# Kernel tuning notes

Hardware: AMD Instinct MI355X
Metric: run time of the kernel (lower is better)

## Reference

```python
import jax, jax.numpy as jnp
import numpy as np

B, S, F, H, A = 256, 128, 512, 1024, 18


def setup_inputs() -> dict:
    key = jax.random.key(0)
    ks = jax.random.split(key, 16)
    u = lambda k, shape, fan: jax.random.uniform(k, shape, jnp.float32, -1.0, 1.0) / np.sqrt(fan)
    return {
        "obs": jax.random.normal(ks[0], (B, S, F), jnp.float32),
        "hx": jax.random.normal(ks[1], (B, H), jnp.float32),
        "cx": jax.random.normal(ks[2], (B, H), jnp.float32),
        "behaviour_acts": jax.random.randint(ks[3], (B, S, 1), 0, A),
        "W1": u(ks[4], (H, F), F), "b1": u(ks[5], (H,), F),
        "W_ih": u(ks[6], (4 * H, H), H), "b_ih": u(ks[7], (4 * H,), H),
        "W_hh": u(ks[8], (4 * H, H), H), "b_hh": u(ks[9], (4 * H,), H),
        "W_v": u(ks[10], (1, H), H), "b_v": u(ks[11], (1,), H),
        "W_l": u(ks[12], (A, H), H), "b_l": u(ks[13], (A,), H),
    }


def reference(obs, hx, cx, behaviour_acts, W1, b1, W_ih, b_ih, W_hh, b_hh, W_v, b_v, W_l, b_l):
    # MLP body: [B,S,F] -> [B,S,H]
    x = jax.nn.relu(jnp.einsum("bsf,hf->bsh", obs, W1) + b1)
    # precompute input-to-gate projection for all timesteps (one big GEMM)
    xg = jnp.einsum("bsh,gh->bsg", x, W_ih) + b_ih  # [B,S,4H]

    def step(carry, xg_t):
        h, c = carry
        gates = xg_t + h @ W_hh.T + b_hh  # [B,4H], gate order i,f,g,o (torch LSTMCell)
        i, f, g, o = jnp.split(gates, 4, axis=-1)
        c = jax.nn.sigmoid(f) * c + jax.nn.sigmoid(i) * jnp.tanh(g)
        h = jax.nn.sigmoid(o) * jnp.tanh(c)
        return (h, c), h

    _, hs = jax.lax.scan(step, (hx, cx), jnp.swapaxes(xg, 0, 1))
    output = jnp.swapaxes(hs, 0, 1)  # [B,S,H]

    value = output @ W_v.T + b_v  # [B,S,1]
    logits = output @ W_l.T + b_l  # [B,S,A]
    # torch Categorical(probs=softmax(logits)) => log-prob via log_softmax
    logp = jax.nn.log_softmax(logits, axis=-1)
    acts = behaviour_acts.reshape(logits.shape[0], logits.shape[1], 1)
    log_probs = jnp.take_along_axis(logp, acts, axis=-1)  # [B,S,1]
    entropy = -jnp.sum(jnp.exp(logp) * logp, axis=-1, keepdims=True)  # [B,S,1]
    return log_probs, entropy, value
```

## Files before the change

kernel.cpp:

```cpp
#include <hip/hip_runtime.h>

#define B_ 256
#define S_ 128
#define F_ 512
#define H_ 1024
#define A_ 18
#define M_ (B_*S_)
#define G_ (4*H_)
#define CH_ 16
#define CR_ (B_*CH_)

typedef unsigned short u16;
typedef __attribute__((ext_vector_type(8))) _Float16 f16x8;
typedef __attribute__((ext_vector_type(4))) _Float16 f16x4;
typedef __attribute__((ext_vector_type(8))) short   s16x8;
typedef __attribute__((ext_vector_type(4))) float f32x4;
typedef __attribute__((ext_vector_type(4))) unsigned int u32x4;

__device__ __forceinline__ float bf2f(u16 u){
  union{unsigned int i; float f;} v; v.i=((unsigned int)u)<<16; return v.f;
}
__device__ __forceinline__ u16 f2bf(float f){
  unsigned int i=__float_as_uint(f);
  unsigned int r=(i+0x7fffu+((i>>16)&1u))>>16;
  return (u16)r;
}
__device__ __forceinline__ u16 f2h(float f){
  _Float16 h=(_Float16)f;
  union{_Float16 h; u16 u;} v; v.h=h; return v.u;
}
__device__ __forceinline__ float ldf(const void* p, size_t i, int m){
  return m ? ((const float*)p)[i] : bf2f(((const u16*)p)[i]);
}
__device__ __forceinline__ f16x8 load8_h(const void* base, size_t off, int m){
  f16x8 v;
  if(m==2) return *(const f16x8*)((const u16*)base + off);
  if(m==1){
    const float* f=(const float*)base + off;
    float4 a=*(const float4*)f; float4 b=*(const float4*)(f+4);
    v[0]=(_Float16)a.x; v[1]=(_Float16)a.y; v[2]=(_Float16)a.z; v[3]=(_Float16)a.w;
    v[4]=(_Float16)b.x; v[5]=(_Float16)b.y; v[6]=(_Float16)b.z; v[7]=(_Float16)b.w;
    return v;
  }
  s16x8 w=*(const s16x8*)((const u16*)base + off);
#pragma unroll
  for(int k=0;k<8;k++) v[k]=(_Float16)bf2f((u16)w[k]);
  return v;
}

__device__ __forceinline__ u32x4 load_c16(const void* p){
  u32x4 r;
  asm volatile("global_load_dwordx4 %0, %1, off sc0 sc1" : "=v"(r) : "v"(p));
  return r;
}
__device__ __forceinline__ void store_c2(u16* p, u16 v){
  unsigned int vv=v;
  asm volatile("global_store_short %0, %1, off sc0 sc1" :: "v"(p), "v"(vv) : "memory");
}
__device__ __forceinline__ int load_c4(const int* p){
  int r;
  asm volatile("global_load_dword %0, %1, off sc0 sc1" : "=v"(r) : "v"(p));
  return r;
}
__device__ __forceinline__ void store_c4(int* p, int v){
  asm volatile("global_store_dword %0, %1, off sc0 sc1" :: "v"(p), "v"(v) : "memory");
}

__device__ __forceinline__ void bar_flags32(int* flags, int target, int gi, int lane, int w){
  asm volatile("s_waitcnt vmcnt(0)" ::: "memory");
  __syncthreads();
  if(w==0){
    if(lane==0) store_c4(flags+gi, target);
    while(true){
      int v=load_c4(flags+(lane&31));
      asm volatile("s_waitcnt vmcnt(0)" ::: "memory");
      if(__all(v>=target)) break;
      __builtin_amdgcn_s_sleep(1);
    }
  }
  __syncthreads();
}

template<int ROWS, int MAP>
__device__ __forceinline__ void stage(const void* base, int mode, int lda, int k0,
                                      int rowoff, int t0, u16* lds, int tid){
  if(mode==2){
    constexpr int NI=(ROWS*8)/256;
    int wv=tid>>6, l=tid&63;
#pragma unroll
    for(int i=0;i<NI;i++){
      int s0=i*256+(wv<<6), s=s0+l;
      int r=s>>3, gc=(s&7)^(r&7);
      int p=rowoff+r, sr;
      if(MAP==0)      sr=p;
      else if(MAP==1) sr=(p&3)*H_+(p>>2);
      else            sr=(p>>4)*S_+t0+(p&15);
      const u16* src=(const u16*)base + (size_t)sr*lda + k0 + gc*8;
      u16* dst=lds + s0*8;
      __builtin_amdgcn_global_load_lds((const __attribute__((address_space(1))) unsigned int*)src,
                                       (__attribute__((address_space(3))) unsigned int*)dst,
                                       16, 0, 0);
    }
  } else {
#pragma unroll
    for(int s0=tid; s0<ROWS*8; s0+=256){
      int r=s0>>3, gc=s0&7, lc=gc^(r&7);
      int p=rowoff+r, sr;
      if(MAP==0)      sr=p;
      else if(MAP==1) sr=(p&3)*H_+(p>>2);
      else            sr=(p>>4)*S_+t0+(p&15);
      f16x8 v=load8_h(base, (size_t)sr*lda + k0 + gc*8, mode);
      *(f16x8*)(lds + r*64 + lc*8)=v;
    }
  }
}

__device__ __forceinline__ f16x8 frag_ld(const u16* lds, int r0, int kc, int lane){
  int r = r0 + (lane&15);
  int c = (kc + (lane>>4)) ^ (r&7);
  return *(const f16x8*)(lds + r*64 + c*8);
}

template<int AMAP, int BMAP, int OUTMODE>
__global__ __launch_bounds__(256,3) void gemm128(const void* A, const void* Bt, void* C,
    const float* __restrict__ biasf, const int* __restrict__ flag,
    int K, int lda, int ldb, int ldc, int t0, int amode, int bmode){
  int m=*flag;
  int am = amode<0 ? m : amode;
  int bm_ = bmode<0 ? m : bmode;
  __shared__ u16 As[128*64];
  __shared__ u16 Bs[128*64];
  int tid=threadIdx.x, lane=tid&63, w=tid>>6;
  int bm=blockIdx.y*128, bn=blockIdx.x*128;
  int wm=(w&1)*64, wn=(w>>1)*64;
  f32x4 acc[4][4];
#pragma unroll
  for(int i=0;i<4;i++)
#pragma unroll
    for(int j=0;j<4;j++) acc[i][j]=(f32x4)(0.f);
  for(int k0=0;k0<K;k0+=64){
    stage<128,AMAP>(A , am,  lda, k0, bm, t0, As, tid);
    stage<128,BMAP>(Bt, bm_, ldb, k0, bn, t0, Bs, tid);
    __syncthreads();
#pragma unroll
    for(int kk=0;kk<2;kk++){
      f16x8 af[4], bq[4];
#pragma unroll
      for(int i=0;i<4;i++) af[i]=frag_ld(As, wm+i*16, kk*4, lane);
#pragma unroll
      for(int j=0;j<4;j++) bq[j]=frag_ld(Bs, wn+j*16, kk*4, lane);
#pragma unroll
      for(int i=0;i<4;i++)
#pragma unroll
        for(int j=0;j<4;j++)
          acc[i][j]=__builtin_amdgcn_mfma_f32_16x16x32_f16(af[i],bq[j],acc[i][j],0,0,0);
    }
    __syncthreads();
  }
  int rl=lane>>4, cl=lane&15;
#pragma unroll
  for(int j=0;j<4;j++){
    int col=bn+wn+j*16+cl;
    float bb=biasf[col];
#pragma unroll
    for(int i=0;i<4;i++){
#pragma unroll
      for(int r=0;r<4;r++){
        int row=bm+wm+i*16+rl*4+r;
        float v=acc[i][j][r]+bb;
        if(OUTMODE==0){ v=fmaxf(v,0.f); ((u16*)C)[(size_t)row*ldc+col]=f2h(v); }
        else if(OUTMODE==2){ ((u16*)C)[(size_t)row*ldc+col]=f2h(v); }
        else { ((float*)C)[(size_t)row*ldc+col]=v; }
      }
    }
  }
}

__global__ __launch_bounds__(512,2) void lstm_persist(u16* __restrict__ hh,
        const u16* __restrict__ Whhp, const u16* __restrict__ xgp,
        float* __restrict__ cst, int* __restrict__ cntc, int tbase){
  __shared__ u16 As[16*2048];
  __shared__ float gs[32*132];
  int tid=threadIdx.x, lane=tid&63, w=tid>>6;
  int grp=blockIdx.x&7, ci=blockIdx.x>>3;
  int bm=grp*32, bn=ci*128;
  int* flags = cntc + grp*64;

  f16x8 bw[32];
#pragma unroll
  for(int t=0;t<32;t++){
    int p = bn + w*16 + (lane&15);
    int k = t*32 + (lane>>4)*8;
    bw[t]=*(const f16x8*)(Whhp + (size_t)p*H_ + k);
  }
#pragma unroll
  for(int t=0;t<32;t++) asm volatile("" : "+a"(bw[t]));

  int rl0=tid>>5, rl1=(tid+512)>>5, u0=tid&31;
  int gu=(bn>>2)+u0;
  float c0=cst[(size_t)(bm+rl0)*H_+gu];
  float c1=cst[(size_t)(bm+rl1)*H_+gu];

  for(int dt=0;dt<CH_;dt++){
    f16x4 xv0=*(const f16x4*)(xgp + ((size_t)(bm+rl0)*CH_+dt)*G_ + bn + u0*4);
    f16x4 xv1=*(const f16x4*)(xgp + ((size_t)(bm+rl1)*CH_+dt)*G_ + bn + u0*4);
    if(dt) bar_flags32(flags, tbase+dt, ci, lane, w);
    {
      int slotPrev=(dt+CH_-1)&(CH_-1);
      u32x4 tmp[8];
#pragma unroll
      for(int i=0;i<8;i++){
        int s=tid+i*512, kt=s>>8, r=(s>>3)&31, gc=s&7;
        tmp[i]=load_c16(hh + ((size_t)(bm+r)*CH_+slotPrev)*H_ + kt*64 + gc*8);
      }
      asm volatile("s_waitcnt vmcnt(0)" ::: "memory");
#pragma unroll
      for(int i=0;i<8;i++){
        int s=tid+i*512, kt=s>>8, r=(s>>3)&31, gc=s&7, lc=gc^(r&7);
        *(u32x4*)(As + kt*2048 + r*64 + lc*8)=tmp[i];
      }
    }
    __syncthreads();
    f32x4 acc0=(f32x4)(0.f), acc1=(f32x4)(0.f);
#pragma unroll
    for(int t=0;t<32;t++){
      int kt=t>>1, kk=t&1;
      f16x8 af0=frag_ld(As+kt*2048, 0,  kk*4, lane);
      f16x8 af1=frag_ld(As+kt*2048, 16, kk*4, lane);
      acc0=__builtin_amdgcn_mfma_f32_16x16x32_f16(af0,bw[t],acc0,0,0,0);
      acc1=__builtin_amdgcn_mfma_f32_16x16x32_f16(af1,bw[t],acc1,0,0,0);
    }
#pragma unroll
    for(int r=0;r<4;r++){
      gs[(   (lane>>4)*4+r)*132 + w*16+(lane&15)]=acc0[r];
      gs[(16+(lane>>4)*4+r)*132 + w*16+(lane&15)]=acc1[r];
    }
    __syncthreads();
    {
      float4 gv=*(const float4*)&gs[rl0*132+u0*4];
      float ii=1.f/(1.f+__expf(-(gv.x+(float)xv0[0])));
      float ff=1.f/(1.f+__expf(-(gv.y+(float)xv0[1])));
      float gg=1.f-2.f/(__expf(2.f*(gv.z+(float)xv0[2]))+1.f);
      float oo=1.f/(1.f+__expf(-(gv.w+(float)xv0[3])));
      c0=ff*c0+ii*gg;
      float th=1.f-2.f/(__expf(2.f*c0)+1.f);
      store_c2(hh + ((size_t)(bm+rl0)*CH_+dt)*H_ + gu, f2h(oo*th));
    }
    {
      float4 gv=*(const float4*)&gs[rl1*132+u0*4];
      float ii=1.f/(1.f+__expf(-(gv.x+(float)xv1[0])));
      float ff=1.f/(1.f+__expf(-(gv.y+(float)xv1[1])));
      float gg=1.f-2.f/(__expf(2.f*(gv.z+(float)xv1[2]))+1.f);
      float oo=1.f/(1.f+__expf(-(gv.w+(float)xv1[3])));
      c1=ff*c1+ii*gg;
      float th=1.f-2.f/(__expf(2.f*c1)+1.f);
      store_c2(hh + ((size_t)(bm+rl1)*CH_+dt)*H_ + gu, f2h(oo*th));
    }
  }
  cst[(size_t)(bm+rl0)*H_+gu]=c0;
  cst[(size_t)(bm+rl1)*H_+gu]=c1;
}

__global__ __launch_bounds__(256,2) void lstm_step(u16* __restrict__ hh, int slotPrev, int dt,
        const void* __restrict__ Whh, const u16* __restrict__ xg,
        float* __restrict__ cst, const int* __restrict__ flag){
  int m=*flag;
  __shared__ u16 As[64*64];
  __shared__ u16 Bs[64*64];
  __shared__ float gs[64*64];
  int tid=threadIdx.x, lane=tid&63, w=tid>>6;
  int bm=blockIdx.y*64, bn=blockIdx.x*64;
  int wm=(w&1)*32, wn=(w>>1)*32;
  f32x4 acc[2][2];
#pragma unroll
  for(int i=0;i<2;i++)
#pragma unroll
    for(int j=0;j<2;j++) acc[i][j]=(f32x4)(0.f);
  for(int k0=0;k0<H_;k0+=64){
    stage<64,0>(hh + slotPrev*H_, 2, CH_*H_, k0, bm, 0, As, tid);
    stage<64,1>(Whh,              m, H_,     k0, bn, 0, Bs, tid);
    __syncthreads();
#pragma unroll
    for(int kk=0;kk<2;kk++){
      f16x8 af[2], bq[2];
#pragma unroll
      for(int i=0;i<2;i++) af[i]=frag_ld(As, wm+i*16, kk*4, lane);
#pragma unroll
      for(int j=0;j<2;j++) bq[j]=frag_ld(Bs, wn+j*16, kk*4, lane);
#pragma unroll
      for(int i=0;i<2;i++)
#pragma unroll
        for(int j=0;j<2;j++)
          acc[i][j]=__builtin_amdgcn_mfma_f32_16x16x32_f16(af[i],bq[j],acc[i][j],0,0,0);
    }
    __syncthreads();
  }
  int rl=lane>>4, cl=lane&15;
#pragma unroll
  for(int j=0;j<2;j++){
    int coll=wn+j*16+cl;
#pragma unroll
    for(int i=0;i<2;i++){
#pragma unroll
      for(int r=0;r<4;r++){
        int rowl=wm+i*16+rl*4+r;
        float xv=(float)((const _Float16*)xg)[((size_t)(bm+rowl)*CH_+dt)*G_ + bn+coll];
        gs[rowl*64+coll]=acc[i][j][r] + xv;
      }
    }
  }
  __syncthreads();
#pragma unroll
  for(int p=0;p<4;p++){
    int idx=p*256+tid;
    int rowl=idx>>4, u=idx&15;
    float4 gv = *(const float4*)&gs[rowl*64+u*4];
    float ii=1.f/(1.f+__expf(-gv.x));
    float ff=1.f/(1.f+__expf(-gv.y));
    float gg=1.f-2.f/(__expf(2.f*gv.z)+1.f);
    float oo=1.f/(1.f+__expf(-gv.w));
    int gb=bm+rowl;
    int gu=(bn>>2)+u;
    size_t ci=(size_t)gb*H_+gu;
    float cn=ff*cst[ci]+ii*gg;
    cst[ci]=cn;
    float th=1.f-2.f/(__expf(2.f*cn)+1.f);
    hh[(size_t)gb*(CH_*H_) + dt*H_ + gu]=f2h(oo*th);
  }
}

__global__ __launch_bounds__(256,2) void heads_chunk(const u16* __restrict__ hh,
      const void* __restrict__ Wl, const void* __restrict__ Wv,
      const float* __restrict__ blf, const int* __restrict__ acts,
      void* __restrict__ out, const int* __restrict__ flag, int t0){
  int m=*flag;
  int rg = blockIdx.x*4 + (threadIdx.x>>6);
  int lane = threadIdx.x & 63;
  const u16* h = hh + (size_t)rg*H_;
  u32x4 hv0=load_c16(h + lane*16);
  u32x4 hv1=load_c16(h + lane*16 + 8);
  f16x8 h0=__builtin_bit_cast(f16x8,hv0), h1=__builtin_bit_cast(f16x8,hv1);
  float hv[16];
#pragma unroll
  for(int k=0;k<8;k++){ hv[k]=(float)h0[k]; hv[8+k]=(float)h1[k]; }
  float dots[19];
#pragma unroll
  for(int j=0;j<19;j++){
    const void* wrow = (j<18) ? Wl : Wv;
    size_t roff = (j<18) ? (size_t)j*H_ : 0;
    float wv_[16];
    if(m){
      const float* f=(const float*)wrow + roff + lane*16;
      float4 a=*(const float4*)f, b=*(const float4*)(f+4), c=*(const float4*)(f+8), d=*(const float4*)(f+12);
      wv_[0]=a.x;wv_[1]=a.y;wv_[2]=a.z;wv_[3]=a.w; wv_[4]=b.x;wv_[5]=b.y;wv_[6]=b.z;wv_[7]=b.w;
      wv_[8]=c.x;wv_[9]=c.y;wv_[10]=c.z;wv_[11]=c.w; wv_[12]=d.x;wv_[13]=d.y;wv_[14]=d.z;wv_[15]=d.w;
    } else {
      const u16* ub=(const u16*)wrow + roff + lane*16;
      s16x8 w0=*(const s16x8*)ub, w1=*(const s16x8*)(ub+8);
#pragma unroll
      for(int k=0;k<8;k++){ wv_[k]=bf2f((u16)w0[k]); wv_[8+k]=bf2f((u16)w1[k]); }
    }
    float d=0.f;
#pragma unroll
    for(int k=0;k<16;k++) d += hv[k]*wv_[k];
#pragma unroll
    for(int mm=1;mm<64;mm<<=1) d += __shfl_xor(d, mm, 64);
    dots[j]=d;
  }
  float lg[18];
#pragma unroll
  for(int j=0;j<18;j++) lg[j]=dots[j]+blf[j];
  float value=dots[18]+blf[18];
  float mx=lg[0];
#pragma unroll
  for(int j=1;j<18;j++) mx=fmaxf(mx,lg[j]);
  float se=0.f, s1=0.f;
#pragma unroll
  for(int j=0;j<18;j++){ float e=__expf(lg[j]-mx); se+=e; s1+=e*(lg[j]-mx); }
  float lse=__logf(se);
  int b=rg>>4, dt=rg&(CH_-1);
  int gw = b*S_ + t0 + dt;
  int a=acts[gw];
  float la=0.f;
#pragma unroll
  for(int j=0;j<18;j++) la = (j==a) ? lg[j] : la;
  float lp=la-mx-lse;
  float ent=lse - s1/se;
  if(lane==0){
    if(m){
      ((float*)out)[gw]=lp; ((float*)out)[M_+gw]=ent; ((float*)out)[2*M_+gw]=value;
    } else {
      ((u16*)out)[gw]=f2bf(lp); ((u16*)out)[M_+gw]=f2bf(ent); ((u16*)out)[2*M_+gw]=f2bf(value);
    }
  }
}

__global__ void detect(const u16* __restrict__ obs_w, int* __restrict__ flag){
  __shared__ float red[256];
  float mx=0.f;
  for(int i=threadIdx.x;i<4096;i+=256) mx=fmaxf(mx,fabsf(bf2f(obs_w[i])));
  red[threadIdx.x]=mx; __syncthreads();
  for(int s=128;s>0;s>>=1){
    if(threadIdx.x<s) red[threadIdx.x]=fmaxf(red[threadIdx.x],red[threadIdx.x+s]);
    __syncthreads();
  }
  if(threadIdx.x==0) *flag=(red[0]>1e4f)?1:0;
}

__global__ void prep(const void* bih, const void* bhh, const void* b1, const void* bl, const void* bv,
                     const void* cx, const void* hx,
                     float* biasg, float* b1f, float* blf, float* cst, u16* hh,
                     int* cnt, const int* __restrict__ flag){
  int m=*flag;
  size_t i=(size_t)blockIdx.x*256+threadIdx.x;
  if(i<G_){ size_t rm=(i&3)*H_+(i>>2); biasg[i]=ldf(bih,rm,m)+ldf(bhh,rm,m); return; }
  i-=G_;
  if(i<H_){ b1f[i]=ldf(b1,i,m); return; }
  i-=H_;
  if(i<19){ blf[i]=(i<18)?ldf(bl,i,m):ldf(bv,0,m); return; }
  i-=19;
  if(i<512){ cnt[i]=0; return; }
  i-=512;
  if(i<(size_t)B_*H_){ cst[i]=ldf(cx,i,m); return; }
  i-=(size_t)B_*H_;
  if(i<(size_t)B_*H_){
    size_t b=i>>10, k=i&1023;
    hh[b*(CH_*H_) + (CH_-1)*H_ + k]=f2h(ldf(hx,i,m));
  }
}

__global__ void convw(const void* W1, const void* Wih, const void* Whh,
                      u16* W1h, u16* Wihp, u16* Whhp, const int* __restrict__ flag){
  int m=*flag;
  size_t i=((size_t)blockIdx.x*256+threadIdx.x)*8;
  const size_t n1=(size_t)H_*F_, n2=(size_t)G_*H_;
  if(i<n1){ *(f16x8*)(W1h+i)=load8_h(W1,i,m); return; }
  i-=n1;
  if(i<n2){ size_t p=i>>10, c=i&1023; size_t sr=(p&3)*H_+(p>>2);
            *(f16x8*)(Wihp+i)=load8_h(Wih, sr*H_+c, m); return; }
  i-=n2;
  if(i<n2){ size_t p=i>>10, c=i&1023; size_t sr=(p&3)*H_+(p>>2);
            *(f16x8*)(Whhp+i)=load8_h(Whh, sr*H_+c, m); return; }
}
__global__ void convobs(const void* obs, u16* obsh, const int* __restrict__ flag){
  int m=*flag;
  size_t i=((size_t)blockIdx.x*256+threadIdx.x)*8;
  if(i<(size_t)M_*F_) *(f16x8*)(obsh+i)=load8_h(obs,i,m);
}

extern "C" void kernel_launch(void* const* d_in, const int* in_sizes, int n_in,
                              void* d_out, int out_size, void* d_ws, size_t ws_size,
                              hipStream_t stream){
  const void* obs=d_in[0];
  const void* hx =d_in[1];
  const void* cx =d_in[2];
  const int* acts=(const int*)d_in[3];
  const void* W1 =d_in[4];
  const void* b1 =d_in[5];
  const void* Wih=d_in[6];
  const void* bih=d_in[7];
  const void* Whh=d_in[8];
  const void* bhh=d_in[9];
  const void* Wv =d_in[10];
  const void* bv =d_in[11];
  const void* Wl =d_in[12];
  const void* bl =d_in[13];

  char* w=(char*)d_ws;
  auto alloc=[&](size_t n){ char* p=w; w+=((n+255)&~(size_t)255); return p; };
  int*   flag =(int*)alloc(4);
  int*   cnt  =(int*)alloc(512*4);
  float* biasg=(float*)alloc((size_t)G_*4);
  float* b1f  =(float*)alloc((size_t)H_*4);
  float* blf  =(float*)alloc(32*4);
  float* cst  =(float*)alloc((size_t)B_*H_*4);
  u16*   hh   =(u16*)alloc((size_t)B_*CH_*H_*2);
  u16*   xc   =(u16*)alloc((size_t)CR_*H_*2);
  u16*   xg   =(u16*)alloc((size_t)CR_*G_*2);
  size_t nW=((size_t)H_*F_ + 2*(size_t)G_*H_)*2 + 768;
  bool pathW = ((size_t)(w-(char*)d_ws) + nW) <= ws_size;
  u16 *W1h=0,*Wihp=0,*Whhp=0;
  if(pathW){ W1h=(u16*)alloc((size_t)H_*F_*2); Wihp=(u16*)alloc((size_t)G_*H_*2); Whhp=(u16*)alloc((size_t)G_*H_*2); }
  size_t nXC=(size_t)M_*H_*2 + 256;
  bool pathXC = pathW && (((size_t)(w-(char*)d_ws) + nXC) <= ws_size);
  u16* xcf=0; if(pathXC) xcf=(u16*)alloc((size_t)M_*H_*2);
  size_t nO=(size_t)M_*F_*2 + 256;
  bool pathO = pathXC && (((size_t)(w-(char*)d_ws) + nO) <= ws_size);
  u16* obsh=0; if(pathO) obsh=(u16*)alloc((size_t)M_*F_*2);

  detect<<<1,256,0,stream>>>((const u16*)obs, flag);
  {
    int total=G_+H_+19+512+B_*H_+B_*H_;
    prep<<<(total+255)/256,256,0,stream>>>(bih,bhh,b1,bl,bv,cx,hx, biasg,b1f,blf,cst,hh,cnt, flag);
  }
  if(pathW){
    size_t n=((size_t)H_*F_+2*(size_t)G_*H_)/8;
    convw<<<(int)((n+255)/256),256,0,stream>>>(W1,Wih,Whh, W1h,Wihp,Whhp, flag);
  }
  if(pathO){
    size_t n=(size_t)M_*F_/8;
    convobs<<<(int)((n+255)/256),256,0,stream>>>(obs, obsh, flag);
  }
  if(pathXC){
    gemm128<0,0,0><<<dim3(H_/128, M_/128),256,0,stream>>>(
        pathO?(const void*)obsh:obs, pathW?(const void*)W1h:W1, xcf, b1f, flag,
        F_, F_, F_, H_, 0, pathO?2:-1, pathW?2:-1);
  }

  for(int c=0;c<S_/CH_;c++){
    int t0=c*CH_;
    if(!pathXC){
      gemm128<2,0,0><<<dim3(H_/128, CR_/128),256,0,stream>>>(
          obs, pathW?(const void*)W1h:W1, xc, b1f, flag, F_, F_, F_, H_, t0, -1, pathW?2:-1);
    }
    if(pathXC)
      gemm128<2,0,2><<<dim3(G_/128, CR_/128),256,0,stream>>>(
          xcf, Wihp, xg, biasg, flag, H_, H_, H_, G_, t0, 2, 2);
    else if(pathW)
      gemm128<0,0,2><<<dim3(G_/128, CR_/128),256,0,stream>>>(
          xc, Wihp, xg, biasg, flag, H_, H_, H_, G_, 0, 2, 2);
    else
      gemm128<0,1,2><<<dim3(G_/128, CR_/128),256,0,stream>>>(
          xc, Wih, xg, biasg, flag, H_, H_, H_, G_, 0, 2, -1);

    if(pathW)
      lstm_persist<<<256,512,0,stream>>>(hh, Whhp, xg, cst, cnt, t0);
    else
      for(int dt=0;dt<CH_;dt++)
        lstm_step<<<dim3(G_/64, B_/64),256,0,stream>>>(hh, (dt+CH_-1)&(CH_-1), dt, Whh, xg, cst, flag);

    heads_chunk<<<dim3(CR_/4),256,0,stream>>>(hh, Wl, Wv, blf, acts, d_out, flag, t0);
  }
}
```

Measured before the change: 1.220 ms.

## Reorganize persistent LSTM step: register gate layout, split barrier, prefetch xg

The MFMA operand order is swapped so each lane's accumulator holds the four gates of one hidden unit. This removes the LDS round trip through the gate buffer and one block barrier per timestep. The grid barrier is split: each block publishes its flag right after storing its h slice, and waits on the others only at the top of the next step. The next step's xg values are prefetched after the flag is published. The h loads now use ordinary cached loads instead of sc0/sc1 coherent loads, with even/odd accumulators added for MFMA ILP. The cost is an extra small LDS transpose before the h stores, and a risk that plain loads read stale h values from other blocks.

```diff
diff --git a/kernel.cpp b/kernel.cpp
--- a/kernel.cpp
+++ b/kernel.cpp
@@ -64,21 +64,6 @@
 }
 __device__ __forceinline__ void store_c4(int* p, int v){
   asm volatile("global_store_dword %0, %1, off sc0 sc1" :: "v"(p), "v"(v) : "memory");
-}
-
-__device__ __forceinline__ void bar_flags32(int* flags, int target, int gi, int lane, int w){
-  asm volatile("s_waitcnt vmcnt(0)" ::: "memory");
-  __syncthreads();
-  if(w==0){
-    if(lane==0) store_c4(flags+gi, target);
-    while(true){
-      int v=load_c4(flags+(lane&31));
-      asm volatile("s_waitcnt vmcnt(0)" ::: "memory");
-      if(__all(v>=target)) break;
-      __builtin_amdgcn_s_sleep(1);
-    }
-  }
-  __syncthreads();
 }
 
 template<int ROWS, int MAP>
@@ -180,7 +165,7 @@
         const u16* __restrict__ Whhp, const u16* __restrict__ xgp,
         float* __restrict__ cst, int* __restrict__ cntc, int tbase){
   __shared__ u16 As[16*2048];
-  __shared__ float gs[32*132];
+  __shared__ u16 hs[32*36];
   int tid=threadIdx.x, lane=tid&63, w=tid>>6;
   int grp=blockIdx.x&7, ci=blockIdx.x>>3;
   int bm=grp*32, bn=ci*128;
@@ -196,24 +181,40 @@
 #pragma unroll
   for(int t=0;t<32;t++) asm volatile("" : "+a"(bw[t]));
 
-  int rl0=tid>>5, rl1=(tid+512)>>5, u0=tid&31;
-  int gu=(bn>>2)+u0;
-  float c0=cst[(size_t)(bm+rl0)*H_+gu];
-  float c1=cst[(size_t)(bm+rl1)*H_+gu];
+  int bb0=lane&15, bb1=16+(lane&15);
+  int ul = w*4 + (lane>>4);
+  int gu2 = (bn>>2) + ul;
+  float c0=cst[(size_t)(bm+bb0)*H_+gu2];
+  float c1=cst[(size_t)(bm+bb1)*H_+gu2];
+  int sb0=tid>>5, su=tid&31, sb1=(tid+512)>>5;
+
+  size_t xoff0=((size_t)(bm+bb0)*CH_)*G_ + bn + w*16 + (lane>>4)*4;
+  size_t xoff1=((size_t)(bm+bb1)*CH_)*G_ + bn + w*16 + (lane>>4)*4;
+  f16x4 xga0=*(const f16x4*)(xgp + xoff0);
+  f16x4 xga1=*(const f16x4*)(xgp + xoff1);
 
   for(int dt=0;dt<CH_;dt++){
-    f16x4 xv0=*(const f16x4*)(xgp + ((size_t)(bm+rl0)*CH_+dt)*G_ + bn + u0*4);
-    f16x4 xv1=*(const f16x4*)(xgp + ((size_t)(bm+rl1)*CH_+dt)*G_ + bn + u0*4);
-    if(dt) bar_flags32(flags, tbase+dt, ci, lane, w);
+    if(dt){
+      if(w==0){
+        int target=tbase+dt;
+        while(true){
+          int v=load_c4(flags+(lane&31));
+          asm volatile("s_waitcnt vmcnt(0)" ::: "memory");
+          if(__all(v>=target)) break;
+          __builtin_amdgcn_s_sleep(1);
+        }
+      }
+      __syncthreads();
+    }
     {
       int slotPrev=(dt+CH_-1)&(CH_-1);
+      const u16* hbase = hh + (size_t)slotPrev*H_;
       u32x4 tmp[8];
 #pragma unroll
       for(int i=0;i<8;i++){
         int s=tid+i*512, kt=s>>8, r=(s>>3)&31, gc=s&7;
-        tmp[i]=load_c16(hh + ((size_t)(bm+r)*CH_+slotPrev)*H_ + kt*64 + gc*8);
+        tmp[i]=*(const u32x4*)(hbase + (size_t)(bm+r)*(CH_*H_) + kt*64 + gc*8);
       }
-      asm volatile("s_waitcnt vmcnt(0)" ::: "memory");
 #pragma unroll
       for(int i=0;i<8;i++){
         int s=tid+i*512, kt=s>>8, r=(s>>3)&31, gc=s&7, lc=gc^(r&7);
@@ -221,44 +222,53 @@
       }
     }
     __syncthreads();
-    f32x4 acc0=(f32x4)(0.f), acc1=(f32x4)(0.f);
-#pragma unroll
-    for(int t=0;t<32;t++){
-      int kt=t>>1, kk=t&1;
-      f16x8 af0=frag_ld(As+kt*2048, 0,  kk*4, lane);
-      f16x8 af1=frag_ld(As+kt*2048, 16, kk*4, lane);
-      acc0=__builtin_amdgcn_mfma_f32_16x16x32_f16(af0,bw[t],acc0,0,0,0);
-      acc1=__builtin_amdgcn_mfma_f32_16x16x32_f16(af1,bw[t],acc1,0,0,0);
-    }
-#pragma unroll
-    for(int r=0;r<4;r++){
-      gs[(   (lane>>4)*4+r)*132 + w*16+(lane&15)]=acc0[r];
-      gs[(16+(lane>>4)*4+r)*132 + w*16+(lane&15)]=acc1[r];
-    }
-    __syncthreads();
+    f32x4 a0e=(f32x4)(0.f), a0o=(f32x4)(0.f), a1e=(f32x4)(0.f), a1o=(f32x4)(0.f);
+#pragma unroll
+    for(int kt=0;kt<16;kt++){
+      f16x8 af0=frag_ld(As+kt*2048, 0,  0, lane);
+      f16x8 af1=frag_ld(As+kt*2048, 16, 0, lane);
+      a0e=__builtin_amdgcn_mfma_f32_16x16x32_f16(bw[2*kt],af0,a0e,0,0,0);
+      a1e=__builtin_amdgcn_mfma_f32_16x16x32_f16(bw[2*kt],af1,a1e,0,0,0);
+      f16x8 bf0=frag_ld(As+kt*2048, 0,  4, lane);
+      f16x8 bf1=frag_ld(As+kt*2048, 16, 4, lane);
+      a0o=__builtin_amdgcn_mfma_f32_16x16x32_f16(bw[2*kt+1],bf0,a0o,0,0,0);
+      a1o=__builtin_amdgcn_mfma_f32_16x16x32_f16(bw[2*kt+1],bf1,a1o,0,0,0);
+    }
+    f32x4 A0=a0e+a0o, A1=a1e+a1o;
+    u16 h0w, h1w;
     {
-      float4 gv=*(const float4*)&gs[rl0*132+u0*4];
-      float ii=1.f/(1.f+__expf(-(gv.x+(float)xv0[0])));
-      float ff=1.f/(1.f+__expf(-(gv.y+(float)xv0[1])));
-      float gg=1.f-2.f/(__expf(2.f*(gv.z+(float)xv0[2]))+1.f);
-      float oo=1.f/(1.f+__expf(-(gv.w+(float)xv0[3])));
+      float ii=1.f/(1.f+__expf(-(A0[0]+(float)xga0[0])));
+      float ff=1.f/(1.f+__expf(-(A0[1]+(float)xga0[1])));
+      float gg=1.f-2.f/(__expf(2.f*(A0[2]+(float)xga0[2]))+1.f);
+      float oo=1.f/(1.f+__expf(-(A0[3]+(float)xga0[3])));
       c0=ff*c0+ii*gg;
       float th=1.f-2.f/(__expf(2.f*c0)+1.f);
-      store_c2(hh + ((size_t)(bm+rl0)*CH_+dt)*H_ + gu, f2h(oo*th));
+      h0w=f2h(oo*th);
     }
     {
-      float4 gv=*(const float4*)&gs[rl1*132+u0*4];
-      float ii=1.f/(1.f+__expf(-(gv.x+(float)xv1[0])));
-      float ff=1.f/(1.f+__expf(-(gv.y+(float)xv1[1])));
-      float gg=1.f-2.f/(__expf(2.f*(gv.z+(float)xv1[2]))+1.f);
-      float oo=1.f/(1.f+__expf(-(gv.w+(float)xv1[3])));
+      float ii=1.f/(1.f+__expf(-(A1[0]+(float)xga1[0])));
+      float ff=1.f/(1.f+__expf(-(A1[1]+(float)xga1[1])));
+      float gg=1.f-2.f/(__expf(2.f*(A1[2]+(float)xga1[2]))+1.f);
+      float oo=1.f/(1.f+__expf(-(A1[3]+(float)xga1[3])));
       c1=ff*c1+ii*gg;
       float th=1.f-2.f/(__expf(2.f*c1)+1.f);
-      store_c2(hh + ((size_t)(bm+rl1)*CH_+dt)*H_ + gu, f2h(oo*th));
-    }
-  }
-  cst[(size_t)(bm+rl0)*H_+gu]=c0;
-  cst[(size_t)(bm+rl1)*H_+gu]=c1;
+      h1w=f2h(oo*th);
+    }
+    hs[bb0*36+ul]=h0w;
+    hs[bb1*36+ul]=h1w;
+    __syncthreads();
+    store_c2(hh + ((size_t)(bm+sb0)*CH_+dt)*H_ + (bn>>2)+su, hs[sb0*36+su]);
+    store_c2(hh + ((size_t)(bm+sb1)*CH_+dt)*H_ + (bn>>2)+su, hs[sb1*36+su]);
+    if(dt<CH_-1){
+      asm volatile("s_waitcnt vmcnt(0)" ::: "memory");
+      __syncthreads();
+      if(tid==0) store_c4(flags+ci, tbase+dt+1);
+      xga0=*(const f16x4*)(xgp + xoff0 + (size_t)(dt+1)*G_);
+      xga1=*(const f16x4*)(xgp + xoff1 + (size_t)(dt+1)*G_);
+    }
+  }
+  cst[(size_t)(bm+bb0)*H_+gu2]=c0;
+  cst[(size_t)(bm+bb1)*H_+gu2]=c1;
 }
 
 __global__ __launch_bounds__(256,2) void lstm_step(u16* __restrict__ hh, int slotPrev, int dt,
```

Result: no change. 1.219 ms (-0.0%).
